# Kernel optimization log

Measured on AMD Instinct MI355X. Metric: run time of the kernel, lower is better.

Reference implementation:

```python
import jax, jax.numpy as jnp
import numpy as np

H = 512

def setup_inputs() -> dict:
    key = jax.random.key(0)
    k1, k2, k3 = jax.random.split(key, 3)
    encoder_outputs = jax.random.normal(k1, (32, 4096, H), dtype=jnp.float32)  # (B,T,H)
    W = jax.random.normal(k2, (H, H), dtype=jnp.float32) * (1.0 / np.sqrt(H))  # attn.weight
    v = jax.random.normal(k3, (H,), dtype=jnp.float32) * (1.0 / np.sqrt(H))    # v param
    return {"encoder_outputs": encoder_outputs, "W": W, "v": v}

def reference(encoder_outputs, W, v):
    # score: energy = tanh(x @ W.T); attn_energies = v . energy over H -> (B,T)
    energy = jnp.tanh(jnp.einsum('bth,gh->btg', encoder_outputs, W))
    attn_energies = jnp.einsum('btg,g->bt', energy, v)
    # method == 'bmm': softmax over T, weighted sum over T -> (B,H)
    attn_w = jax.nn.softmax(attn_energies, axis=-1)
    out = jnp.einsum('bt,bth->bh', attn_w, encoder_outputs)
    return out
```

## Files before the change

### kernel.cpp

```cpp
#include <hip/hip_runtime.h>
#include <hip/hip_bf16.h>

typedef __attribute__((ext_vector_type(8))) short short8;
typedef __attribute__((ext_vector_type(4))) float f32x4;

#define B_SZ 32
#define T_SZ 4096
#define H_SZ 512
#define NROWS (B_SZ * T_SZ)

static __device__ __forceinline__ unsigned int pack2(float a, float b) {
  unsigned int r;
  asm("v_cvt_pk_bf16_f32 %0, %1, %2" : "=v"(r) : "v"(a), "v"(b));
  return r;
}

static __device__ __forceinline__ float fast_tanh(float x) {
  float e = __expf(2.0f * x);
  return 1.0f - 2.0f / (e + 1.0f);
}

__global__ __launch_bounds__(256) void prep_w_kernel(
    const float* __restrict__ W, uint4* __restrict__ Wfrag) {
  int s = blockIdx.x * 256 + threadIdx.x;
  int grow  = s >> 6;
  int kt    = (s >> 2) & 15;
  int kslot = s & 3;
  const float4* Wf4 = reinterpret_cast<const float4*>(W);
  float4 lo = Wf4[grow * 128 + kt * 8 + kslot * 2];
  float4 hi = Wf4[grow * 128 + kt * 8 + kslot * 2 + 1];
  uint4 u;
  u.x = pack2(lo.x, lo.y); u.y = pack2(lo.z, lo.w);
  u.z = pack2(hi.x, hi.y); u.w = pack2(hi.z, hi.w);
  int nb = grow >> 4, g = grow & 15;
  Wfrag[nb * 1024 + kt * 64 + kslot * 16 + g] = u;
}

__global__ __launch_bounds__(256, 2) void score_fused_kernel(
    const float* __restrict__ X, const uint4* __restrict__ Wfrag,
    const float* __restrict__ v,
    float* __restrict__ num, float2* __restrict__ md) {
  __shared__ unsigned char WsB[3][16384];
  __shared__ float vLDS[512];
  __shared__ float sLDS[128];
  __shared__ float pLDS[128];
  __shared__ float mred[2], dred[2];

  const int tid   = threadIdx.x;
  const int lane  = tid & 63;
  const int wave  = tid >> 6;
  const int frow  = lane & 15;
  const int kslot = lane >> 4;
  const size_t rowbase = (size_t)blockIdx.x * 128;

  #define STAGE_RD(c, p)                                                        \
    {                                                                           \
      const char* src = (const char*)Wfrag + (size_t)(c) * 16384 +              \
                        (p) * 4096 + wave * 1024 + lane * 16;                   \
      unsigned char* dst = &WsB[(c) % 3][(p) * 4096 + wave * 1024];             \
      __builtin_amdgcn_global_load_lds((const unsigned int*)src,                \
                                       (unsigned int*)dst, 16, 0, 0);           \
    }

  #pragma unroll
  for (int p = 0; p < 4; ++p) STAGE_RD(0, p);
  #pragma unroll
  for (int p = 0; p < 4; ++p) STAGE_RD(1, p);
  reinterpret_cast<float2*>(vLDS)[tid] = reinterpret_cast<const float2*>(v)[tid];

  short8 afrag0[16], afrag1[16];
  {
    const float4* xr0 = reinterpret_cast<const float4*>(X + (rowbase + wave * 32 + frow) * H_SZ);
    const float4* xr1 = reinterpret_cast<const float4*>(X + (rowbase + wave * 32 + 16 + frow) * H_SZ);
    #pragma unroll
    for (int kt = 0; kt < 16; ++kt) {
      float4 lo0 = xr0[kt * 8 + kslot * 2];
      float4 hi0 = xr0[kt * 8 + kslot * 2 + 1];
      union { uint4 u; short8 s; } c0;
      c0.u.x = pack2(lo0.x, lo0.y); c0.u.y = pack2(lo0.z, lo0.w);
      c0.u.z = pack2(hi0.x, hi0.y); c0.u.w = pack2(hi0.z, hi0.w);
      afrag0[kt] = c0.s;
      float4 lo1 = xr1[kt * 8 + kslot * 2];
      float4 hi1 = xr1[kt * 8 + kslot * 2 + 1];
      union { uint4 u; short8 s; } c1;
      c1.u.x = pack2(lo1.x, lo1.y); c1.u.y = pack2(lo1.z, lo1.w);
      c1.u.z = pack2(hi1.x, hi1.y); c1.u.w = pack2(hi1.z, hi1.w);
      afrag1[kt] = c1.s;
    }
  }
  asm volatile("s_waitcnt vmcnt(4) lgkmcnt(0)" ::: "memory");
  __builtin_amdgcn_s_barrier();
  __builtin_amdgcn_sched_barrier(0);

  float red0[4] = {0.f, 0.f, 0.f, 0.f};
  float red1[4] = {0.f, 0.f, 0.f, 0.f};

  for (int ch = 0; ch < 32; ++ch) {
    const int stage_c = ch + 2;
    const unsigned char* bb = &WsB[ch % 3][lane * 16];
    float vg = vLDS[ch * 16 + frow];

    f32x4 acc[2][2];
    #pragma unroll
    for (int a = 0; a < 2; ++a)
      #pragma unroll
      for (int p = 0; p < 2; ++p)
        acc[a][p] = (f32x4){0.f, 0.f, 0.f, 0.f};

    #pragma unroll
    for (int ph = 0; ph < 4; ++ph) {
      short8 b0 = *reinterpret_cast<const short8*>(bb + (ph * 4 + 0) * 1024);
      short8 b1 = *reinterpret_cast<const short8*>(bb + (ph * 4 + 1) * 1024);
      short8 b2 = *reinterpret_cast<const short8*>(bb + (ph * 4 + 2) * 1024);
      short8 b3 = *reinterpret_cast<const short8*>(bb + (ph * 4 + 3) * 1024);
      if (stage_c < 32) STAGE_RD(stage_c, ph);
      __builtin_amdgcn_s_barrier();
      __builtin_amdgcn_sched_barrier(0);
      __builtin_amdgcn_s_setprio(1);
      {
        const int k0 = ph * 4;
        acc[0][(k0 + 0) & 1] = __builtin_amdgcn_mfma_f32_16x16x32_bf16(afrag0[k0 + 0], b0, acc[0][(k0 + 0) & 1], 0, 0, 0);
        acc[1][(k0 + 0) & 1] = __builtin_amdgcn_mfma_f32_16x16x32_bf16(afrag1[k0 + 0], b0, acc[1][(k0 + 0) & 1], 0, 0, 0);
        acc[0][(k0 + 1) & 1] = __builtin_amdgcn_mfma_f32_16x16x32_bf16(afrag0[k0 + 1], b1, acc[0][(k0 + 1) & 1], 0, 0, 0);
        acc[1][(k0 + 1) & 1] = __builtin_amdgcn_mfma_f32_16x16x32_bf16(afrag1[k0 + 1], b1, acc[1][(k0 + 1) & 1], 0, 0, 0);
        acc[0][(k0 + 2) & 1] = __builtin_amdgcn_mfma_f32_16x16x32_bf16(afrag0[k0 + 2], b2, acc[0][(k0 + 2) & 1], 0, 0, 0);
        acc[1][(k0 + 2) & 1] = __builtin_amdgcn_mfma_f32_16x16x32_bf16(afrag1[k0 + 2], b2, acc[1][(k0 + 2) & 1], 0, 0, 0);
        acc[0][(k0 + 3) & 1] = __builtin_amdgcn_mfma_f32_16x16x32_bf16(afrag0[k0 + 3], b3, acc[0][(k0 + 3) & 1], 0, 0, 0);
        acc[1][(k0 + 3) & 1] = __builtin_amdgcn_mfma_f32_16x16x32_bf16(afrag1[k0 + 3], b3, acc[1][(k0 + 3) & 1], 0, 0, 0);
      }
      __builtin_amdgcn_s_setprio(0);
      __builtin_amdgcn_s_barrier();
      __builtin_amdgcn_sched_barrier(0);
    }

    #pragma unroll
    for (int r = 0; r < 4; ++r) {
      red0[r] = fmaf(vg, fast_tanh(acc[0][0][r] + acc[0][1][r]), red0[r]);
      red1[r] = fmaf(vg, fast_tanh(acc[1][0][r] + acc[1][1][r]), red1[r]);
    }

    if (ch < 31) {
      if (ch < 30) {
        asm volatile("s_waitcnt vmcnt(4)" ::: "memory");
      } else {
        asm volatile("s_waitcnt vmcnt(0)" ::: "memory");
      }
      __builtin_amdgcn_s_barrier();
      __builtin_amdgcn_sched_barrier(0);
    }
  }
  #undef STAGE_RD

  #pragma unroll
  for (int r = 0; r < 4; ++r) {
    #pragma unroll
    for (int d = 1; d < 16; d <<= 1) {
      red0[r] += __shfl_xor(red0[r], d);
      red1[r] += __shfl_xor(red1[r], d);
    }
  }
  if (frow == 0) {
    float* sp = sLDS + wave * 32 + kslot * 4;
    sp[0]  = red0[0]; sp[1]  = red0[1]; sp[2]  = red0[2]; sp[3]  = red0[3];
    sp[16] = red1[0]; sp[17] = red1[1]; sp[18] = red1[2]; sp[19] = red1[3];
  }
  __syncthreads();

  if (tid < 128) {
    float s = sLDS[tid];
    float m = s;
    #pragma unroll
    for (int d = 1; d < 64; d <<= 1) m = fmaxf(m, __shfl_xor(m, d));
    if ((tid & 63) == 0) mred[tid >> 6] = m;
  }
  __syncthreads();
  const float m_loc = fmaxf(mred[0], mred[1]);
  if (tid < 128) {
    float p = __expf(sLDS[tid] - m_loc);
    pLDS[tid] = p;
    #pragma unroll
    for (int d = 1; d < 64; d <<= 1) p += __shfl_xor(p, d);
    if ((tid & 63) == 0) dred[tid >> 6] = p;
  }
  __syncthreads();

  {
    float ax = 0.f, ay = 0.f;
    const float2* xb = reinterpret_cast<const float2*>(X + rowbase * H_SZ) + tid;
    #pragma unroll 8
    for (int t = 0; t < 128; ++t) {
      float p = pLDS[t];
      float2 xv = xb[(size_t)t * (H_SZ / 2)];
      ax = fmaf(p, xv.x, ax);
      ay = fmaf(p, xv.y, ay);
    }
    float2 r; r.x = ax; r.y = ay;
    reinterpret_cast<float2*>(num + (size_t)blockIdx.x * H_SZ)[tid] = r;
  }
  if (tid == 0) {
    float2 r; r.x = m_loc; r.y = dred[0] + dred[1];
    md[blockIdx.x] = r;
  }
}

__global__ __launch_bounds__(512) void combine_kernel(
    const float* __restrict__ num, const float2* __restrict__ md,
    float* __restrict__ out) {
  const int b = blockIdx.x;
  const int h = threadIdx.x;
  float M = -1e30f;
  #pragma unroll
  for (int c = 0; c < 32; ++c) M = fmaxf(M, md[b * 32 + c].x);
  float den = 0.f, acc = 0.f;
  #pragma unroll 4
  for (int c = 0; c < 32; ++c) {
    float2 m2 = md[b * 32 + c];
    float w = __expf(m2.x - M);
    den += w * m2.y;
    acc = fmaf(w, num[(size_t)(b * 32 + c) * H_SZ + h], acc);
  }
  out[b * H_SZ + h] = acc / den;
}

extern "C" void kernel_launch(void* const* d_in, const int* in_sizes, int n_in,
                              void* d_out, int out_size, void* d_ws, size_t ws_size,
                              hipStream_t stream) {
  const float* X = (const float*)d_in[0];
  const float* W = (const float*)d_in[1];
  const float* v = (const float*)d_in[2];
  float* out = (float*)d_out;
  unsigned char* ws = (unsigned char*)d_ws;

  uint4* Wfrag = (uint4*)(ws);
  float* num   = (float*)(ws + (512u << 10));
  float2* md   = (float2*)(ws + (512u << 10) + (2u << 20));

  prep_w_kernel<<<128, 256, 0, stream>>>(W, Wfrag);
  score_fused_kernel<<<NROWS / 128, 256, 0, stream>>>(X, Wfrag, v, num, md);
  combine_kernel<<<B_SZ, 512, 0, stream>>>(num, md, out);
}
```

Before: 163.6 us.

## Replace triple-buffered W staging with single 64KB chunk load per 64 columns

Drops the 3-stage rolling LDS pipeline for W fragments. The kernel now loads a 64 KB chunk covering 64 output columns, waits on it fully, and then runs 16 k-steps of 8 independent MFMAs across 4 accumulators per row block. The aim is fewer barriers and waitcnts per chunk and more independent MFMA chains. The trade-off is no overlap between the W loads and compute, and a larger LDS footprint that may reduce occupancy. v is now read directly from global memory instead of LDS, and prep_w lays out Wfrag to match the new chunk order.

```diff
diff --git a/kernel.cpp b/kernel.cpp
--- a/kernel.cpp
+++ b/kernel.cpp
@@ -14,7 +14,6 @@
   asm("v_cvt_pk_bf16_f32 %0, %1, %2" : "=v"(r) : "v"(a), "v"(b));
   return r;
 }
-
 static __device__ __forceinline__ float fast_tanh(float x) {
   float e = __expf(2.0f * x);
   return 1.0f - 2.0f / (e + 1.0f);
@@ -23,25 +22,27 @@
 __global__ __launch_bounds__(256) void prep_w_kernel(
     const float* __restrict__ W, uint4* __restrict__ Wfrag) {
   int s = blockIdx.x * 256 + threadIdx.x;
-  int grow  = s >> 6;
-  int kt    = (s >> 2) & 15;
-  int kslot = s & 3;
+  int frow  = s & 15;
+  int kslot = (s >> 4) & 3;
+  int kt    = (s >> 6) & 15;
+  int j     = (s >> 10) & 3;
+  int c     = s >> 12;
+  int g  = c * 64 + j * 16 + frow;
+  int k0 = kt * 32 + kslot * 8;
   const float4* Wf4 = reinterpret_cast<const float4*>(W);
-  float4 lo = Wf4[grow * 128 + kt * 8 + kslot * 2];
-  float4 hi = Wf4[grow * 128 + kt * 8 + kslot * 2 + 1];
+  float4 lo = Wf4[g * 128 + (k0 >> 2)];
+  float4 hi = Wf4[g * 128 + (k0 >> 2) + 1];
   uint4 u;
   u.x = pack2(lo.x, lo.y); u.y = pack2(lo.z, lo.w);
   u.z = pack2(hi.x, hi.y); u.w = pack2(hi.z, hi.w);
-  int nb = grow >> 4, g = grow & 15;
-  Wfrag[nb * 1024 + kt * 64 + kslot * 16 + g] = u;
+  Wfrag[s] = u;
 }
 
 __global__ __launch_bounds__(256, 2) void score_fused_kernel(
     const float* __restrict__ X, const uint4* __restrict__ Wfrag,
     const float* __restrict__ v,
     float* __restrict__ num, float2* __restrict__ md) {
-  __shared__ unsigned char WsB[3][16384];
-  __shared__ float vLDS[512];
+  __shared__ unsigned char WsB[65536];
   __shared__ float sLDS[128];
   __shared__ float pLDS[128];
   __shared__ float mred[2], dred[2];
@@ -52,21 +53,6 @@
   const int frow  = lane & 15;
   const int kslot = lane >> 4;
   const size_t rowbase = (size_t)blockIdx.x * 128;
-
-  #define STAGE_RD(c, p)                                                        \
-    {                                                                           \
-      const char* src = (const char*)Wfrag + (size_t)(c) * 16384 +              \
-                        (p) * 4096 + wave * 1024 + lane * 16;                   \
-      unsigned char* dst = &WsB[(c) % 3][(p) * 4096 + wave * 1024];             \
-      __builtin_amdgcn_global_load_lds((const unsigned int*)src,                \
-                                       (unsigned int*)dst, 16, 0, 0);           \
-    }
-
-  #pragma unroll
-  for (int p = 0; p < 4; ++p) STAGE_RD(0, p);
-  #pragma unroll
-  for (int p = 0; p < 4; ++p) STAGE_RD(1, p);
-  reinterpret_cast<float2*>(vLDS)[tid] = reinterpret_cast<const float2*>(v)[tid];
 
   short8 afrag0[16], afrag1[16];
   {
@@ -88,68 +74,68 @@
       afrag1[kt] = c1.s;
     }
   }
-  asm volatile("s_waitcnt vmcnt(4) lgkmcnt(0)" ::: "memory");
-  __builtin_amdgcn_s_barrier();
-  __builtin_amdgcn_sched_barrier(0);
 
   float red0[4] = {0.f, 0.f, 0.f, 0.f};
   float red1[4] = {0.f, 0.f, 0.f, 0.f};
 
-  for (int ch = 0; ch < 32; ++ch) {
-    const int stage_c = ch + 2;
-    const unsigned char* bb = &WsB[ch % 3][lane * 16];
-    float vg = vLDS[ch * 16 + frow];
-
-    f32x4 acc[2][2];
+  for (int c = 0; c < 8; ++c) {
+    {
+      const char* src = (const char*)Wfrag + (size_t)c * 65536 + tid * 16;
+      unsigned char* dst = WsB + tid * 16;
+      #pragma unroll
+      for (int i = 0; i < 16; ++i)
+        __builtin_amdgcn_global_load_lds((const unsigned int*)(src + i * 4096),
+                                         (unsigned int*)(dst + i * 4096), 16, 0, 0);
+    }
+    float vv0 = v[c * 64 + frow];
+    float vv1 = v[c * 64 + 16 + frow];
+    float vv2 = v[c * 64 + 32 + frow];
+    float vv3 = v[c * 64 + 48 + frow];
+
+    asm volatile("s_waitcnt vmcnt(0)" ::: "memory");
+    __builtin_amdgcn_s_barrier();
+    __builtin_amdgcn_sched_barrier(0);
+
+    f32x4 acc[2][4];
     #pragma unroll
     for (int a = 0; a < 2; ++a)
       #pragma unroll
-      for (int p = 0; p < 2; ++p)
-        acc[a][p] = (f32x4){0.f, 0.f, 0.f, 0.f};
-
-    #pragma unroll
-    for (int ph = 0; ph < 4; ++ph) {
-      short8 b0 = *reinterpret_cast<const short8*>(bb + (ph * 4 + 0) * 1024);
-      short8 b1 = *reinterpret_cast<const short8*>(bb + (ph * 4 + 1) * 1024);
-      short8 b2 = *reinterpret_cast<const short8*>(bb + (ph * 4 + 2) * 1024);
-      short8 b3 = *reinterpret_cast<const short8*>(bb + (ph * 4 + 3) * 1024);
-      if (stage_c < 32) STAGE_RD(stage_c, ph);
-      __builtin_amdgcn_s_barrier();
-      __builtin_amdgcn_sched_barrier(0);
-      __builtin_amdgcn_s_setprio(1);
-      {
-        const int k0 = ph * 4;
-        acc[0][(k0 + 0) & 1] = __builtin_amdgcn_mfma_f32_16x16x32_bf16(afrag0[k0 + 0], b0, acc[0][(k0 + 0) & 1], 0, 0, 0);
-        acc[1][(k0 + 0) & 1] = __builtin_amdgcn_mfma_f32_16x16x32_bf16(afrag1[k0 + 0], b0, acc[1][(k0 + 0) & 1], 0, 0, 0);
-        acc[0][(k0 + 1) & 1] = __builtin_amdgcn_mfma_f32_16x16x32_bf16(afrag0[k0 + 1], b1, acc[0][(k0 + 1) & 1], 0, 0, 0);
-        acc[1][(k0 + 1) & 1] = __builtin_amdgcn_mfma_f32_16x16x32_bf16(afrag1[k0 + 1], b1, acc[1][(k0 + 1) & 1], 0, 0, 0);
-        acc[0][(k0 + 2) & 1] = __builtin_amdgcn_mfma_f32_16x16x32_bf16(afrag0[k0 + 2], b2, acc[0][(k0 + 2) & 1], 0, 0, 0);
-        acc[1][(k0 + 2) & 1] = __builtin_amdgcn_mfma_f32_16x16x32_bf16(afrag1[k0 + 2], b2, acc[1][(k0 + 2) & 1], 0, 0, 0);
-        acc[0][(k0 + 3) & 1] = __builtin_amdgcn_mfma_f32_16x16x32_bf16(afrag0[k0 + 3], b3, acc[0][(k0 + 3) & 1], 0, 0, 0);
-        acc[1][(k0 + 3) & 1] = __builtin_amdgcn_mfma_f32_16x16x32_bf16(afrag1[k0 + 3], b3, acc[1][(k0 + 3) & 1], 0, 0, 0);
-      }
-      __builtin_amdgcn_s_setprio(0);
-      __builtin_amdgcn_s_barrier();
-      __builtin_amdgcn_sched_barrier(0);
-    }
+      for (int j = 0; j < 4; ++j)
+        acc[a][j] = (f32x4){0.f, 0.f, 0.f, 0.f};
+
+    const unsigned char* bb = WsB + lane * 16;
+    __builtin_amdgcn_s_setprio(1);
+    #pragma unroll
+    for (int kt = 0; kt < 16; ++kt) {
+      short8 b0 = *reinterpret_cast<const short8*>(bb + (0 * 16 + kt) * 1024);
+      short8 b1 = *reinterpret_cast<const short8*>(bb + (1 * 16 + kt) * 1024);
+      short8 b2 = *reinterpret_cast<const short8*>(bb + (2 * 16 + kt) * 1024);
+      short8 b3 = *reinterpret_cast<const short8*>(bb + (3 * 16 + kt) * 1024);
+      acc[0][0] = __builtin_amdgcn_mfma_f32_16x16x32_bf16(afrag0[kt], b0, acc[0][0], 0, 0, 0);
+      acc[1][0] = __builtin_amdgcn_mfma_f32_16x16x32_bf16(afrag1[kt], b0, acc[1][0], 0, 0, 0);
+      acc[0][1] = __builtin_amdgcn_mfma_f32_16x16x32_bf16(afrag0[kt], b1, acc[0][1], 0, 0, 0);
+      acc[1][1] = __builtin_amdgcn_mfma_f32_16x16x32_bf16(afrag1[kt], b1, acc[1][1], 0, 0, 0);
+      acc[0][2] = __builtin_amdgcn_mfma_f32_16x16x32_bf16(afrag0[kt], b2, acc[0][2], 0, 0, 0);
+      acc[1][2] = __builtin_amdgcn_mfma_f32_16x16x32_bf16(afrag1[kt], b2, acc[1][2], 0, 0, 0);
+      acc[0][3] = __builtin_amdgcn_mfma_f32_16x16x32_bf16(afrag0[kt], b3, acc[0][3], 0, 0, 0);
+      acc[1][3] = __builtin_amdgcn_mfma_f32_16x16x32_bf16(afrag1[kt], b3, acc[1][3], 0, 0, 0);
+    }
+    __builtin_amdgcn_s_setprio(0);
 
     #pragma unroll
     for (int r = 0; r < 4; ++r) {
-      red0[r] = fmaf(vg, fast_tanh(acc[0][0][r] + acc[0][1][r]), red0[r]);
-      red1[r] = fmaf(vg, fast_tanh(acc[1][0][r] + acc[1][1][r]), red1[r]);
-    }
-
-    if (ch < 31) {
-      if (ch < 30) {
-        asm volatile("s_waitcnt vmcnt(4)" ::: "memory");
-      } else {
-        asm volatile("s_waitcnt vmcnt(0)" ::: "memory");
-      }
-      __builtin_amdgcn_s_barrier();
-      __builtin_amdgcn_sched_barrier(0);
-    }
-  }
-  #undef STAGE_RD
+      red0[r] = fmaf(vv0, fast_tanh(acc[0][0][r]), red0[r]);
+      red0[r] = fmaf(vv1, fast_tanh(acc[0][1][r]), red0[r]);
+      red0[r] = fmaf(vv2, fast_tanh(acc[0][2][r]), red0[r]);
+      red0[r] = fmaf(vv3, fast_tanh(acc[0][3][r]), red0[r]);
+      red1[r] = fmaf(vv0, fast_tanh(acc[1][0][r]), red1[r]);
+      red1[r] = fmaf(vv1, fast_tanh(acc[1][1][r]), red1[r]);
+      red1[r] = fmaf(vv2, fast_tanh(acc[1][2][r]), red1[r]);
+      red1[r] = fmaf(vv3, fast_tanh(acc[1][3][r]), red1[r]);
+    }
+
+    __builtin_amdgcn_s_barrier();
+  }
 
   #pragma unroll
   for (int r = 0; r < 4; ++r) {
```

Result: faster. 138.6 us (-15.3%).
